# Kernel optimization log

Measured on AMD Instinct MI355X. Metric: run time of the kernel, lower is better.

Reference implementation:

```python
import jax, jax.numpy as jnp
import numpy as np

B, S, D = 2, 2048, 4096
H, KV, HD = 32, 8, 128
THETA = 10000.0


def rotate_half(x):
    x1, x2 = x[..., : HD // 2], x[..., HD // 2 :]
    return jnp.concatenate((-x2, x1), axis=-1)


def setup_inputs() -> dict:
    key = jax.random.key(0)
    ks = jax.random.split(key, 8)
    s = 1.0 / np.sqrt(D)
    return {
        "hidden_states": jax.random.normal(ks[0], (B, S, D), jnp.float32),
        "modality_indicators": jax.random.randint(ks[1], (B, S), 0, 2, jnp.int64 if jax.config.jax_enable_x64 else jnp.int32),
        "position_ids": jnp.arange(S, dtype=jnp.int32),
        "Wq": jax.random.normal(ks[2], (D, H * HD), jnp.float32) * s,
        "Wk0": jax.random.normal(ks[3], (D, KV * HD), jnp.float32) * s,
        "Wk1": jax.random.normal(ks[4], (D, KV * HD), jnp.float32) * s,
        "Wv0": jax.random.normal(ks[5], (D, KV * HD), jnp.float32) * s,
        "Wv1": jax.random.normal(ks[6], (D, KV * HD), jnp.float32) * s,
        "Wo": jax.random.normal(ks[7], (H * HD, D), jnp.float32) * s,
    }


def reference(hidden_states, modality_indicators, position_ids, Wq, Wk0, Wk1, Wv0, Wv1, Wo):
    x = hidden_states
    # Multiway (modality-routed) k/v projections: per-token select between two linears.
    sel = (modality_indicators == 1)[..., None]  # [B,S,1]
    q = x @ Wq                                   # [B,S,H*HD]
    k = jnp.where(sel, x @ Wk1, x @ Wk0)         # [B,S,KV*HD]
    v = jnp.where(sel, x @ Wv1, x @ Wv0)

    q = q.reshape(B, S, H, HD).transpose(0, 2, 1, 3)    # [B,H,S,HD]
    k = k.reshape(B, S, KV, HD).transpose(0, 2, 1, 3)   # [B,KV,S,HD]
    v = v.reshape(B, S, KV, HD).transpose(0, 2, 1, 3)

    # RoPE cache and application (emb = cat(freqs, freqs))
    inv_freq = 1.0 / (THETA ** (jnp.arange(0, HD, 2, dtype=jnp.float32) / HD))
    freqs = position_ids.astype(jnp.float32)[:, None] * inv_freq[None, :]   # [S,HD/2]
    emb = jnp.concatenate((freqs, freqs), axis=-1)                          # [S,HD]
    cos = jnp.cos(emb)[None, None, :, :]                                    # [1,1,S,HD]
    sin = jnp.sin(emb)[None, None, :, :]
    q = q * cos + rotate_half(q) * sin
    k = k * cos + rotate_half(k) * sin

    # GQA: repeat kv heads
    n_rep = H // KV
    k = jnp.repeat(k, n_rep, axis=1)  # [B,H,S,HD]
    v = jnp.repeat(v, n_rep, axis=1)

    scores = jnp.einsum("bhqd,bhkd->bhqk", q, k) / np.sqrt(HD)
    causal = jnp.tril(jnp.ones((S, S), dtype=bool))
    scores = jnp.where(causal[None, None], scores, jnp.finfo(scores.dtype).min)
    attn = jax.nn.softmax(scores, axis=-1)
    ctx = jnp.einsum("bhqk,bhkd->bhqd", attn, v)            # [B,H,S,HD]
    ctx = ctx.transpose(0, 2, 1, 3).reshape(B, S, H * HD)
    return ctx @ Wo
```

## Files before the change

### kernel.cpp

```cpp
#include <hip/hip_runtime.h>

typedef unsigned short u16;
typedef unsigned int   u32;
using bf16x8 = __attribute__((ext_vector_type(8))) __bf16;
using f32x4  = __attribute__((ext_vector_type(4))) float;
using f32x16 = __attribute__((ext_vector_type(16))) float;
using u32x4  = __attribute__((ext_vector_type(4))) unsigned int;


__device__ __forceinline__ u16 f2bf(float f) {
  u32 u = __builtin_bit_cast(u32, f);
  return (u16)((u + 0x7fffu + ((u >> 16) & 1u)) >> 16);
}
__device__ __forceinline__ float bf2f(u16 h) {
  return __builtin_bit_cast(float, (u32)h << 16);
}
__device__ __forceinline__ f32x4 mfma16(bf16x8 a, bf16x8 b, f32x4 c) {
  return __builtin_amdgcn_mfma_f32_16x16x32_bf16(a, b, c, 0, 0, 0);
}
__device__ __forceinline__ f32x16 mfma32(bf16x8 a, bf16x8 b, f32x16 c) {
  return __builtin_amdgcn_mfma_f32_32x32x16_bf16(a, b, c, 0, 0, 0);
}
__device__ __forceinline__ f32x16 zero16() {
  f32x16 z;
#pragma unroll
  for (int i = 0; i < 16; ++i) z[i] = 0.f;
  return z;
}
__device__ __forceinline__ void g2l16(const void* gp, void* lp) {
  __builtin_amdgcn_global_load_lds(
      (__attribute__((address_space(1))) void*)(void*)gp,
      (__attribute__((address_space(3))) void*)lp, 16, 0, 0);
}

__global__ void k_cvt(const float* __restrict__ in, u16* __restrict__ out, int n4) {
  int i = blockIdx.x * 256 + threadIdx.x;
  if (i >= n4) return;
  float4 v = ((const float4*)in)[i];
  ushort4 o;
  o.x = f2bf(v.x); o.y = f2bf(v.y); o.z = f2bf(v.z); o.w = f2bf(v.w);
  ((ushort4*)out)[i] = o;
}

__global__ void k_tcvt(const float* __restrict__ in, u16* __restrict__ out, int K, int N) {
  __shared__ u16 t[32][33];
  int n0 = blockIdx.x * 32, k0 = blockIdx.y * 32;
  int r = threadIdx.x >> 3, c4 = (threadIdx.x & 7) * 4;
  float4 v = *(const float4*)(in + (size_t)(k0 + r) * N + n0 + c4);
  t[c4 + 0][r] = f2bf(v.x);
  t[c4 + 1][r] = f2bf(v.y);
  t[c4 + 2][r] = f2bf(v.z);
  t[c4 + 3][r] = f2bf(v.w);
  __syncthreads();
  ushort4 o;
  o.x = t[r][c4 + 0]; o.y = t[r][c4 + 1]; o.z = t[r][c4 + 2]; o.w = t[r][c4 + 3];
  *(ushort4*)(out + (size_t)(n0 + r) * K + k0 + c4) = o;
}

#define TILE_BODY(T, VMLIT, DOSTAGE)                                         \
  {                                                                          \
    asm volatile("s_waitcnt vmcnt(" VMLIT ")" ::: "memory");                 \
    __builtin_amdgcn_s_barrier();                                            \
    __builtin_amdgcn_sched_barrier(0);                                       \
    const u16* base_ = lds + ((T) & 3) * 16384;                              \
    bf16x8 bfr[4], afr[4];                                                   \
    _Pragma("unroll")                                                        \
    for (int nf = 0; nf < 4; ++nf)                                           \
      bfr[nf] = *(const bf16x8*)(base_ + boff + nf * 512);                   \
    _Pragma("unroll")                                                        \
    for (int mf = 0; mf < 4; ++mf)                                           \
      afr[mf] = *(const bf16x8*)(base_ + aoff + mf * 512);                   \
    if (DOSTAGE) stage((T) + 3);                                             \
    __builtin_amdgcn_s_setprio(1);                                           \
    _Pragma("unroll")                                                        \
    for (int mf = 0; mf < 4; ++mf)                                           \
      _Pragma("unroll")                                                      \
      for (int nf = 0; nf < 4; ++nf)                                         \
        acc[mf][nf] = mfma16(afr[mf], bfr[nf], acc[mf][nf]);                 \
    __builtin_amdgcn_s_setprio(0);                                           \
    _Pragma("unroll")                                                        \
    for (int mf = 0; mf < 4; ++mf)                                           \
      afr[mf] = *(const bf16x8*)(base_ + aoff + (mf + 4) * 512);             \
    __builtin_amdgcn_s_setprio(1);                                           \
    _Pragma("unroll")                                                        \
    for (int mf = 0; mf < 4; ++mf)                                           \
      _Pragma("unroll")                                                      \
      for (int nf = 0; nf < 4; ++nf)                                         \
        acc[mf + 4][nf] = mfma16(afr[mf], bfr[nf], acc[mf + 4][nf]);         \
    __builtin_amdgcn_s_setprio(0);                                           \
  }

template <int MODE>
__global__ __launch_bounds__(512, 2) void k_gemm8(const u16* __restrict__ A, const u16* __restrict__ Bt,
                                                  void* __restrict__ Cp, int NH) {
  __shared__ u16 lds[4 * 16384];
  const int tid = threadIdx.x, wid = tid >> 6, l = tid & 63, g = l >> 4, li = l & 15;
  const int wr = wid >> 2, wc = wid & 3;
  const int bid = blockIdx.x;
  const int swz = (bid & 7) * 32 + (bid >> 3);
  const int m0 = (swz >> 4) * 256, n0 = (swz & 15) * 256;

  const int bo = wid * 2048 + l * 16;
  const int srow = bo >> 6;
  const int sgg = (l & 3) ^ ((l >> 3) & 3);
  const u16* ApA = A + (size_t)(m0 + srow) * 4096 + sgg * 8;
  const u16* ApB = Bt + (size_t)(n0 + srow) * 4096 + sgg * 8;

  auto stage = [&](int t) {
    const u16* a = ApA + t * 32;
    const u16* b = ApB + t * 32;
    u16* da = (u16*)lds + (t & 3) * 16384 + wid * 1024;
    u16* db = da + 8192;
    g2l16(a, da);
    g2l16(a + (size_t)16 * 4096, da + 512);
    g2l16(b, db);
    g2l16(b + (size_t)16 * 4096, db + 512);
  };

  const int lsl8 = (g ^ ((li >> 1) & 3)) * 8;
  const int aoff = (wr * 128 + li) * 32 + lsl8;
  const int boff = 8192 + (wc * 64 + li) * 32 + lsl8;

  const f32x4 vzero = {0.f, 0.f, 0.f, 0.f};
  f32x4 acc[8][4];
#pragma unroll
  for (int m = 0; m < 8; ++m)
#pragma unroll
    for (int n = 0; n < 4; ++n) acc[m][n] = vzero;

  stage(0); stage(1); stage(2);
  for (int t = 0; t < 125; ++t) TILE_BODY(t, "8", true);
  TILE_BODY(125, "8", false);
  TILE_BODY(126, "4", false);
  TILE_BODY(127, "0", false);

  (void)NH;
#pragma unroll
  for (int mf = 0; mf < 8; ++mf)
#pragma unroll
    for (int nf = 0; nf < 4; ++nf)
#pragma unroll
      for (int j = 0; j < 4; ++j) {
        int row = m0 + wr * 128 + mf * 16 + g * 4 + j;
        int col = n0 + wc * 64 + nf * 16 + li;
        float v = acc[mf][nf][j];
        if constexpr (MODE == 2) {
          ((float*)Cp)[(size_t)row * 4096 + col] = v;
        } else if constexpr (MODE == 1) {
          int b = row >> 11, s = row & 2047, h = col >> 7, d = col & 127;
          ((u16*)Cp)[(((size_t)(b * NH + h)) * 2048 + s) * 128 + d] = f2bf(v);
        } else {
          int b = row >> 11, s = row & 2047;
          int buf = col >> 10, hh = (col >> 7) & 7, d = col & 127;
          ((u16*)Cp)[(size_t)buf * 4194304 + (((size_t)(b * 8 + hh)) * 2048 + s) * 128 + d] = f2bf(v);
        }
      }
}

__global__ void k_ropeq(u16* __restrict__ Q, const int* __restrict__ pos) {
  int row = blockIdx.x * 4 + (threadIdx.x >> 6);
  int l = threadIdx.x & 63;
  int s = row & 2047;
  u16* p = Q + (size_t)row * 128;
  float x1 = bf2f(p[l]), x2 = bf2f(p[l + 64]);
  float ang = (float)pos[s] * expf((float)l * -0.14391156831212787f);
  float cs = cosf(ang), sn = sinf(ang);
  const float sc = 0.08838834764831845f;
  p[l] = f2bf((x1 * cs - x2 * sn) * sc);
  p[l + 64] = f2bf((x2 * cs + x1 * sn) * sc);
}

__global__ void k_kvprep(const u16* __restrict__ K0, const u16* __restrict__ K1,
                         const u16* __restrict__ V0, const u16* __restrict__ V1,
                         const int* __restrict__ mod, const int* __restrict__ pos,
                         u16* __restrict__ Kr, u16* __restrict__ Vt) {
  __shared__ u16 Vl[64][136];
  int blk = blockIdx.x;
  int st = blk & 31, kvh = (blk >> 5) & 7, b = blk >> 8;
  int s0 = st * 64;
  int tid = threadIdx.x, wid = tid >> 6, l = tid & 63;
  float invf = expf((float)l * -0.14391156831212787f);
  size_t slab = (size_t)(b * 8 + kvh) * 2048;
  for (int rr = 0; rr < 16; ++rr) {
    int r = wid * 16 + rr;
    int s = s0 + r;
    int sel = mod[b * 2048 + s];
    const u16* ks = (sel ? K1 : K0) + (slab + s) * 128;
    const u16* vs = (sel ? V1 : V0) + (slab + s) * 128;
    float ang = (float)pos[s] * invf;
    float cs = cosf(ang), sn = sinf(ang);
    float x1 = bf2f(ks[l]), x2 = bf2f(ks[l + 64]);
    u16* kd = Kr + (slab + s) * 128;
    kd[l] = f2bf(x1 * cs - x2 * sn);
    kd[l + 64] = f2bf(x2 * cs + x1 * sn);
    Vl[r][l] = vs[l];
    Vl[r][l + 64] = vs[l + 64];
  }
  __syncthreads();
  int d = tid >> 1, si0 = (tid & 1) * 32;
  u16* vd = Vt + ((size_t)(b * 8 + kvh) * 128 + d) * 2048 + s0 + si0;
#pragma unroll
  for (int k4 = 0; k4 < 8; ++k4) {
    ushort4 o;
    o.x = Vl[si0 + k4 * 4 + 0][d];
    o.y = Vl[si0 + k4 * 4 + 1][d];
    o.z = Vl[si0 + k4 * 4 + 2][d];
    o.w = Vl[si0 + k4 * 4 + 3][d];
    *(ushort4*)(vd + k4 * 4) = o;
  }
}

__global__ __launch_bounds__(256, 2) void k_attn(const u16* __restrict__ Q, const u16* __restrict__ Kr,
                                                 const u16* __restrict__ Vt, u16* __restrict__ ctx) {
  __shared__ u16 Kl[2 * 64 * 128];
  __shared__ u16 Vl[2 * 128 * 64];
  const int bh = blockIdx.x;
  const int qi = 15 - (int)blockIdx.y;
  const int b = bh >> 5, h = bh & 31, kvh = h >> 2;
  const int tid = threadIdx.x, w = tid >> 6, l = tid & 63;
  const int lo5 = l & 31, hi = l >> 5;
  const bool hib = hi != 0;
  const int q0 = qi * 128;
  const int qlane = q0 + w * 32 + lo5;
  const size_t kvslab = (size_t)(b * 8 + kvh) * 2048;
  const u16* Kg = Kr + kvslab * 128;
  const u16* Vg = Vt + kvslab * 128;

  auto stage = [&](int kt, int bi) {
#pragma unroll
    for (int i = 0; i < 4; ++i) {
      int c = w * 4 + i;
      int slot = c * 1024 + l * 16;
      {
        int row = slot >> 8;
        int inner = (slot & 255) ^ ((row & 7) << 4);
        g2l16((const char*)Kg + kt * 16384 + row * 256 + inner,
              (char*)Kl + bi * 16384 + c * 1024);
      }
      {
        int row = slot >> 7;
        int inner = (slot & 127) ^ ((row & 7) << 4);
        g2l16((const char*)Vg + (size_t)row * 4096 + kt * 128 + inner,
              (char*)Vl + bi * 16384 + c * 1024);
      }
    }
  };

  const u16* qrow = Q + ((size_t)bh * 2048 + qlane) * 128;
  bf16x8 qf[8];
#pragma unroll
  for (int kk = 0; kk < 8; ++kk) qf[kk] = *(const bf16x8*)(qrow + kk * 16 + hi * 8);

  f32x16 ot[4];
#pragma unroll
  for (int i = 0; i < 4; ++i) ot[i] = zero16();
  float m = -1e30f, ls = 0.f;
  const float L2E = 1.4426950408889634f;

  const int nkt = 2 * qi + 2;
  stage(0, 0);
  __syncthreads();
  int cur = 0;
  for (int kt = 0; kt < nkt; ++kt) {
    if (kt + 1 < nkt) stage(kt + 1, cur ^ 1);
    const char* kbase = (const char*)Kl + cur * 16384;
    const char* vbase = (const char*)Vl + cur * 16384;
    const int ktb = kt * 64;
    if (ktb <= q0 + w * 32 + 31) {
      f32x16 st[2];
      st[0] = zero16(); st[1] = zero16();
#pragma unroll
      for (int kk = 0; kk < 8; ++kk) {
        bf16x8 kfr[2];
#pragma unroll
        for (int mf = 0; mf < 2; ++mf) {
          int row = mf * 32 + lo5;
          kfr[mf] = *(const bf16x8*)(kbase + row * 256 + ((kk * 32 + hi * 16) ^ ((row & 7) << 4)));
        }
        __builtin_amdgcn_s_setprio(1);
        st[0] = mfma32(kfr[0], qf[kk], st[0]);
        st[1] = mfma32(kfr[1], qf[kk], st[1]);
        __builtin_amdgcn_s_setprio(0);
      }
      if (ktb + 63 > q0 + w * 32) {
#pragma unroll
        for (int mf = 0; mf < 2; ++mf)
#pragma unroll
          for (int r = 0; r < 16; ++r) {
            int kg = ktb + mf * 32 + (r & 3) + 8 * (r >> 2) + 4 * hi;
            if (kg > qlane) st[mf][r] = -3.0e38f;
          }
      }
      float t[16];
#pragma unroll
      for (int r = 0; r < 16; ++r) t[r] = fmaxf(st[0][r], st[1][r]);
#pragma unroll
      for (int s = 8; s >= 1; s >>= 1)
#pragma unroll
        for (int r = 0; r < s; ++r) t[r] = fmaxf(t[r], t[r + s]);
      float pmax = fmaxf(t[0], __shfl_xor(t[0], 32));
      if (!__all(pmax <= m + 8.f)) {
        float nm = fmaxf(m, pmax);
        float resc = exp2f((m - nm) * L2E);
        m = nm;
        ls *= resc;
#pragma unroll
        for (int i = 0; i < 4; ++i)
#pragma unroll
          for (int r = 0; r < 16; ++r) ot[i][r] *= resc;
      }
#pragma unroll
      for (int mf = 0; mf < 2; ++mf)
#pragma unroll
        for (int r = 0; r < 16; ++r) st[mf][r] = exp2f((st[mf][r] - m) * L2E);
      float u[16];
#pragma unroll
      for (int r = 0; r < 16; ++r) u[r] = st[0][r] + st[1][r];
#pragma unroll
      for (int s = 8; s >= 1; s >>= 1)
#pragma unroll
        for (int r = 0; r < s; ++r) u[r] += u[r + s];
      ls += u[0] + __shfl_xor(u[0], 32);
      u32 pkv[16];
#pragma unroll
      for (int mf = 0; mf < 2; ++mf)
#pragma unroll
        for (int tt = 0; tt < 8; ++tt) {
          u32 r;
          asm("v_cvt_pk_bf16_f32 %0, %1, %2" : "=v"(r) : "v"(st[mf][2 * tt]), "v"(st[mf][2 * tt + 1]));
          pkv[mf * 8 + tt] = r;
        }
      bf16x8 pfrag[4];
#pragma unroll
      for (int kk = 0; kk < 4; ++kk) {
        int c = (kk >> 1) * 8 + (kk & 1) * 4;
        u32 m0 = hib ? pkv[c + 2] : pkv[c + 0];
        u32 m1 = hib ? pkv[c + 3] : pkv[c + 1];
        u32 s0 = hib ? pkv[c + 0] : pkv[c + 2];
        u32 s1 = hib ? pkv[c + 1] : pkv[c + 3];
        u32 r0 = (u32)__shfl_xor((int)s0, 32);
        u32 r1 = (u32)__shfl_xor((int)s1, 32);
        u32x4 wv = {hib ? r0 : m0, hib ? r1 : m1, hib ? m0 : r0, hib ? m1 : r1};
        pfrag[kk] = __builtin_bit_cast(bf16x8, wv);
      }
#pragma unroll
      for (int mfV = 0; mfV < 4; ++mfV) {
        int row = mfV * 32 + lo5;
        const char* vb = vbase + row * 128;
        int sw = (row & 7) << 4;
        bf16x8 vf[4];
#pragma unroll
        for (int kk = 0; kk < 4; ++kk)
          vf[kk] = *(const bf16x8*)(vb + ((kk * 32 + hi * 16) ^ sw));
        __builtin_amdgcn_s_setprio(1);
#pragma unroll
        for (int kk = 0; kk < 4; ++kk) ot[mfV] = mfma32(vf[kk], pfrag[kk], ot[mfV]);
        __builtin_amdgcn_s_setprio(0);
      }
    }
    __syncthreads();
    cur ^= 1;
  }
  float inv = 1.0f / ls;
  u16* crow = ctx + ((size_t)(b * 2048) + qlane) * 4096 + h * 128;
#pragma unroll
  for (int mfV = 0; mfV < 4; ++mfV)
#pragma unroll
    for (int rq = 0; rq < 4; ++rq) {
      ushort4 o4;
      o4.x = f2bf(ot[mfV][rq * 4 + 0] * inv);
      o4.y = f2bf(ot[mfV][rq * 4 + 1] * inv);
      o4.z = f2bf(ot[mfV][rq * 4 + 2] * inv);
      o4.w = f2bf(ot[mfV][rq * 4 + 3] * inv);
      *(ushort4*)(crow + mfV * 32 + rq * 8 + hi * 4) = o4;
    }
}

extern "C" void kernel_launch(void* const* d_in, const int* in_sizes, int n_in,
                              void* d_out, int out_size, void* d_ws, size_t ws_size,
                              hipStream_t stream) {
  (void)in_sizes; (void)n_in; (void)out_size; (void)ws_size;
  const float* X   = (const float*)d_in[0];
  const int*   mod = (const int*)d_in[1];
  const int*   pos = (const int*)d_in[2];
  const float* Wq  = (const float*)d_in[3];
  const float* Wk0 = (const float*)d_in[4];
  const float* Wk1 = (const float*)d_in[5];
  const float* Wv0 = (const float*)d_in[6];
  const float* Wv1 = (const float*)d_in[7];
  const float* Wo  = (const float*)d_in[8];
  float* out = (float*)d_out;

  u16* p = (u16*)d_ws;
  auto take = [&](size_t n) { u16* r = p; p += n; return r; };
  u16* Xb   = take(16777216);
  u16* WqT  = take(16777216);
  u16* WoT  = take(16777216);
  u16* WkvT = take(16777216);
  u16* Qr   = take(16777216);
  u16* KV4  = take(16777216);
  u16* Kr  = WqT;
  u16* Vtr = WqT + 4194304;
  u16* ctx = Xb;

  k_cvt<<<dim3(16384), 256, 0, stream>>>(X, Xb, 4194304);
  k_tcvt<<<dim3(128, 128), 256, 0, stream>>>(Wq, WqT, 4096, 4096);
  k_tcvt<<<dim3(32, 128), 256, 0, stream>>>(Wk0, WkvT,               4096, 1024);
  k_tcvt<<<dim3(32, 128), 256, 0, stream>>>(Wk1, WkvT + 1 * 4194304, 4096, 1024);
  k_tcvt<<<dim3(32, 128), 256, 0, stream>>>(Wv0, WkvT + 2 * 4194304, 4096, 1024);
  k_tcvt<<<dim3(32, 128), 256, 0, stream>>>(Wv1, WkvT + 3 * 4194304, 4096, 1024);
  k_tcvt<<<dim3(128, 128), 256, 0, stream>>>(Wo, WoT, 4096, 4096);

  k_gemm8<1><<<dim3(256), 512, 0, stream>>>(Xb, WqT,  (void*)Qr,  32);
  k_gemm8<3><<<dim3(256), 512, 0, stream>>>(Xb, WkvT, (void*)KV4, 8);

  k_ropeq<<<dim3(32768), 256, 0, stream>>>(Qr, pos);
  k_kvprep<<<dim3(512), 256, 0, stream>>>(KV4, KV4 + 4194304, KV4 + 2 * 4194304,
                                          KV4 + 3 * 4194304, mod, pos, Kr, Vtr);

  k_attn<<<dim3(64, 16), 256, 0, stream>>>(Qr, Kr, Vtr, ctx);

  k_gemm8<2><<<dim3(256), 512, 0, stream>>>(ctx, WoT, (void*)out, 0);
}
```

Before: 581.5 us.

## Route tokens by modality into grouped KV GEMM and pair causal attention tiles

A prefix-scan kernel builds a per-batch permutation that groups tokens by modality, padded to 256-row tiles. A new grouped GEMM then computes only the selected K/V projection for each token instead of both and discarding half, which roughly halves the K/V projection FLOPs at the cost of gathered row loads and scattered stores. The attention kernel now processes two query tiles per block (p and 15-p) to balance causal work across blocks, halving the grid. The K tile LDS swizzle is also widened to 16 rows.

```diff
diff --git a/kernel.cpp b/kernel.cpp
--- a/kernel.cpp
+++ b/kernel.cpp
@@ -55,6 +55,35 @@
   ushort4 o;
   o.x = t[r][c4 + 0]; o.y = t[r][c4 + 1]; o.z = t[r][c4 + 2]; o.w = t[r][c4 + 3];
   *(ushort4*)(out + (size_t)(n0 + r) * K + k0 + c4) = o;
+}
+
+__global__ void k_scan(const int* __restrict__ mod, int* __restrict__ perm, int* __restrict__ meta) {
+  __shared__ int ps[1024];
+  const int b = blockIdx.x, t = threadIdx.x;
+  perm[b * 2304 + t] = -1;
+  perm[b * 2304 + 1024 + t] = -1;
+  if (t < 256) perm[b * 2304 + 2048 + t] = -1;
+  const int i0 = 2 * t, i1 = 2 * t + 1;
+  const int f0 = (mod[b * 2048 + i0] != 1) ? 1 : 0;
+  const int f1 = (mod[b * 2048 + i1] != 1) ? 1 : 0;
+  const int sum = f0 + f1;
+  ps[t] = sum;
+  __syncthreads();
+  for (int off = 1; off < 1024; off <<= 1) {
+    int v = (t >= off) ? ps[t - off] : 0;
+    __syncthreads();
+    ps[t] += v;
+    __syncthreads();
+  }
+  const int total0 = ps[1023];
+  const int excl = ps[t] - sum;
+  const int nt0 = (total0 + 255) >> 8;
+  const int off1 = nt0 * 256;
+  const int s0 = f0 ? excl : off1 + (i0 - excl);
+  const int s1 = f1 ? (excl + f0) : off1 + (i1 - (excl + f0));
+  perm[b * 2304 + s0] = i0;
+  perm[b * 2304 + s1] = i1;
+  if (t == 0) { meta[b * 2] = total0; meta[b * 2 + 1] = nt0; }
 }
 
 #define TILE_BODY(T, VMLIT, DOSTAGE)                                         \
@@ -149,10 +178,72 @@
         } else if constexpr (MODE == 1) {
           int b = row >> 11, s = row & 2047, h = col >> 7, d = col & 127;
           ((u16*)Cp)[(((size_t)(b * NH + h)) * 2048 + s) * 128 + d] = f2bf(v);
-        } else {
-          int b = row >> 11, s = row & 2047;
-          int buf = col >> 10, hh = (col >> 7) & 7, d = col & 127;
-          ((u16*)Cp)[(size_t)buf * 4194304 + (((size_t)(b * 8 + hh)) * 2048 + s) * 128 + d] = f2bf(v);
+        }
+      }
+}
+
+__global__ __launch_bounds__(512, 2) void k_gemmkv(const u16* __restrict__ Xb,
+                                                   const u16* __restrict__ B0, const u16* __restrict__ B1,
+                                                   const int* __restrict__ perm, const int* __restrict__ meta,
+                                                   u16* __restrict__ Ksel, u16* __restrict__ Vsel) {
+  __shared__ u16 lds[4 * 16384];
+  const int tid = threadIdx.x, wid = tid >> 6, l = tid & 63, g = l >> 4, li = l & 15;
+  const int wr = wid >> 2, wc = wid & 3;
+  const int bb = blockIdx.y / 9, tm = blockIdx.y % 9;
+  const int n0 = blockIdx.x * 256;
+  const int nt0 = meta[bb * 2 + 1];
+  const u16* Bt = (tm >= nt0) ? B1 : B0;
+
+  const int bo = wid * 2048 + l * 16;
+  const int srow = bo >> 6;
+  const int sgg = (l & 3) ^ ((l >> 3) & 3);
+  int t0 = perm[bb * 2304 + tm * 256 + srow];
+  int t1 = perm[bb * 2304 + tm * 256 + srow + 16];
+  if (t0 < 0) t0 = 0;
+  if (t1 < 0) t1 = 0;
+  const u16* ApA0 = Xb + ((size_t)bb * 2048 + t0) * 4096 + sgg * 8;
+  const u16* ApA1 = Xb + ((size_t)bb * 2048 + t1) * 4096 + sgg * 8;
+  const u16* ApB = Bt + (size_t)(n0 + srow) * 4096 + sgg * 8;
+
+  auto stage = [&](int t) {
+    u16* da = (u16*)lds + (t & 3) * 16384 + wid * 1024;
+    u16* db = da + 8192;
+    g2l16(ApA0 + t * 32, da);
+    g2l16(ApA1 + t * 32, da + 512);
+    g2l16(ApB + t * 32, db);
+    g2l16(ApB + (size_t)16 * 4096 + t * 32, db + 512);
+  };
+
+  const int lsl8 = (g ^ ((li >> 1) & 3)) * 8;
+  const int aoff = (wr * 128 + li) * 32 + lsl8;
+  const int boff = 8192 + (wc * 64 + li) * 32 + lsl8;
+
+  const f32x4 vzero = {0.f, 0.f, 0.f, 0.f};
+  f32x4 acc[8][4];
+#pragma unroll
+  for (int m = 0; m < 8; ++m)
+#pragma unroll
+    for (int n = 0; n < 4; ++n) acc[m][n] = vzero;
+
+  stage(0); stage(1); stage(2);
+  for (int t = 0; t < 125; ++t) TILE_BODY(t, "8", true);
+  TILE_BODY(125, "8", false);
+  TILE_BODY(126, "4", false);
+  TILE_BODY(127, "0", false);
+
+#pragma unroll
+  for (int mf = 0; mf < 8; ++mf)
+#pragma unroll
+    for (int nf = 0; nf < 4; ++nf)
+#pragma unroll
+      for (int j = 0; j < 4; ++j) {
+        int slot = tm * 256 + wr * 128 + mf * 16 + g * 4 + j;
+        int tok = perm[bb * 2304 + slot];
+        if (tok >= 0) {
+          int col = n0 + wc * 64 + nf * 16 + li;
+          int kv = col >> 10, hh = (col >> 7) & 7, d = col & 127;
+          u16* dst = (kv ? Vsel : Ksel) + (((size_t)(bb * 8 + hh)) * 2048 + tok) * 128 + d;
+          *dst = f2bf(acc[mf][nf][j]);
         }
       }
 }
@@ -170,9 +261,8 @@
   p[l + 64] = f2bf((x2 * cs + x1 * sn) * sc);
 }
 
-__global__ void k_kvprep(const u16* __restrict__ K0, const u16* __restrict__ K1,
-                         const u16* __restrict__ V0, const u16* __restrict__ V1,
-                         const int* __restrict__ mod, const int* __restrict__ pos,
+__global__ void k_kvprep(const u16* __restrict__ Ks, const u16* __restrict__ Vs,
+                         const int* __restrict__ pos,
                          u16* __restrict__ Kr, u16* __restrict__ Vt) {
   __shared__ u16 Vl[64][136];
   int blk = blockIdx.x;
@@ -184,9 +274,8 @@
   for (int rr = 0; rr < 16; ++rr) {
     int r = wid * 16 + rr;
     int s = s0 + r;
-    int sel = mod[b * 2048 + s];
-    const u16* ks = (sel ? K1 : K0) + (slab + s) * 128;
-    const u16* vs = (sel ? V1 : V0) + (slab + s) * 128;
+    const u16* ks = Ks + (slab + s) * 128;
+    const u16* vs = Vs + (slab + s) * 128;
     float ang = (float)pos[s] * invf;
     float cs = cosf(ang), sn = sinf(ang);
     float x1 = bf2f(ks[l]), x2 = bf2f(ks[l + 64]);
@@ -215,16 +304,15 @@
   __shared__ u16 Kl[2 * 64 * 128];
   __shared__ u16 Vl[2 * 128 * 64];
   const int bh = blockIdx.x;
-  const int qi = 15 - (int)blockIdx.y;
+  const int p = blockIdx.y;
   const int b = bh >> 5, h = bh & 31, kvh = h >> 2;
   const int tid = threadIdx.x, w = tid >> 6, l = tid & 63;
   const int lo5 = l & 31, hi = l >> 5;
   const bool hib = hi != 0;
-  const int q0 = qi * 128;
-  const int qlane = q0 + w * 32 + lo5;
   const size_t kvslab = (size_t)(b * 8 + kvh) * 2048;
   const u16* Kg = Kr + kvslab * 128;
   const u16* Vg = Vt + kvslab * 128;
+  const float L2E = 1.4426950408889634f;
 
   auto stage = [&](int kt, int bi) {
 #pragma unroll
@@ -233,7 +321,7 @@
       int slot = c * 1024 + l * 16;
       {
         int row = slot >> 8;
-        int inner = (slot & 255) ^ ((row & 7) << 4);
+        int inner = (slot & 255) ^ ((row & 15) << 4);
         g2l16((const char*)Kg + kt * 16384 + row * 256 + inner,
               (char*)Kl + bi * 16384 + c * 1024);
       }
@@ -246,134 +334,138 @@
     }
   };
 
-  const u16* qrow = Q + ((size_t)bh * 2048 + qlane) * 128;
-  bf16x8 qf[8];
-#pragma unroll
-  for (int kk = 0; kk < 8; ++kk) qf[kk] = *(const bf16x8*)(qrow + kk * 16 + hi * 8);
-
-  f32x16 ot[4];
-#pragma unroll
-  for (int i = 0; i < 4; ++i) ot[i] = zero16();
-  float m = -1e30f, ls = 0.f;
-  const float L2E = 1.4426950408889634f;
-
-  const int nkt = 2 * qi + 2;
-  stage(0, 0);
-  __syncthreads();
-  int cur = 0;
-  for (int kt = 0; kt < nkt; ++kt) {
-    if (kt + 1 < nkt) stage(kt + 1, cur ^ 1);
-    const char* kbase = (const char*)Kl + cur * 16384;
-    const char* vbase = (const char*)Vl + cur * 16384;
-    const int ktb = kt * 64;
-    if (ktb <= q0 + w * 32 + 31) {
-      f32x16 st[2];
-      st[0] = zero16(); st[1] = zero16();
-#pragma unroll
-      for (int kk = 0; kk < 8; ++kk) {
-        bf16x8 kfr[2];
-#pragma unroll
-        for (int mf = 0; mf < 2; ++mf) {
-          int row = mf * 32 + lo5;
-          kfr[mf] = *(const bf16x8*)(kbase + row * 256 + ((kk * 32 + hi * 16) ^ ((row & 7) << 4)));
-        }
-        __builtin_amdgcn_s_setprio(1);
-        st[0] = mfma32(kfr[0], qf[kk], st[0]);
-        st[1] = mfma32(kfr[1], qf[kk], st[1]);
-        __builtin_amdgcn_s_setprio(0);
+  for (int hf = 0; hf < 2; ++hf) {
+    const int qi = hf ? (15 - p) : p;
+    const int q0 = qi * 128;
+    const int qlane = q0 + w * 32 + lo5;
+    const u16* qrow = Q + ((size_t)bh * 2048 + qlane) * 128;
+    bf16x8 qf[8];
+#pragma unroll
+    for (int kk = 0; kk < 8; ++kk) qf[kk] = *(const bf16x8*)(qrow + kk * 16 + hi * 8);
+
+    f32x16 ot[4];
+#pragma unroll
+    for (int i = 0; i < 4; ++i) ot[i] = zero16();
+    float m = -1e30f, ls = 0.f;
+
+    const int nkt = 2 * qi + 2;
+    stage(0, 0);
+    __syncthreads();
+    int cur = 0;
+    for (int kt = 0; kt < nkt; ++kt) {
+      if (kt + 1 < nkt) stage(kt + 1, cur ^ 1);
+      const char* kbase = (const char*)Kl + cur * 16384;
+      const char* vbase = (const char*)Vl + cur * 16384;
+      const int ktb = kt * 64;
+      if (ktb <= q0 + w * 32 + 31) {
+        f32x16 st[2];
+        st[0] = zero16(); st[1] = zero16();
+#pragma unroll
+        for (int kk = 0; kk < 8; ++kk) {
+          bf16x8 kfr[2];
+#pragma unroll
+          for (int mf = 0; mf < 2; ++mf) {
+            int row = mf * 32 + lo5;
+            kfr[mf] = *(const bf16x8*)(kbase + row * 256 + ((kk * 32 + hi * 16) ^ ((row & 15) << 4)));
+          }
+          __builtin_amdgcn_s_setprio(1);
+          st[0] = mfma32(kfr[0], qf[kk], st[0]);
+          st[1] = mfma32(kfr[1], qf[kk], st[1]);
+          __builtin_amdgcn_s_setprio(0);
+        }
+        if (ktb + 63 > q0 + w * 32) {
+#pragma unroll
+          for (int mf = 0; mf < 2; ++mf)
+#pragma unroll
+            for (int r = 0; r < 16; ++r) {
+              int kg = ktb + mf * 32 + (r & 3) + 8 * (r >> 2) + 4 * hi;
+              if (kg > qlane) st[mf][r] = -3.0e38f;
+            }
+        }
+        float t[16];
+#pragma unroll
+        for (int r = 0; r < 16; ++r) t[r] = fmaxf(st[0][r], st[1][r]);
+#pragma unroll
+        for (int s = 8; s >= 1; s >>= 1)
+#pragma unroll
+          for (int r = 0; r < s; ++r) t[r] = fmaxf(t[r], t[r + s]);
+        float pmax = fmaxf(t[0], __shfl_xor(t[0], 32));
+        if (!__all(pmax <= m + 8.f)) {
+          float nm = fmaxf(m, pmax);
+          float resc = exp2f((m - nm) * L2E);
+          m = nm;
+          ls *= resc;
+#pragma unroll
+          for (int i = 0; i < 4; ++i)
+#pragma unroll
+            for (int r = 0; r < 16; ++r) ot[i][r] *= resc;
+        }
+#pragma unroll
+        for (int mf = 0; mf < 2; ++mf)
+#pragma unroll
+          for (int r = 0; r < 16; ++r) st[mf][r] = exp2f((st[mf][r] - m) * L2E);
+        float u[16];
+#pragma unroll
+        for (int r = 0; r < 16; ++r) u[r] = st[0][r] + st[1][r];
+#pragma unroll
+        for (int s = 8; s >= 1; s >>= 1)
+#pragma unroll
+          for (int r = 0; r < s; ++r) u[r] += u[r + s];
+        ls += u[0] + __shfl_xor(u[0], 32);
+        u32 pkv[16];
+#pragma unroll
+        for (int mf = 0; mf < 2; ++mf)
+#pragma unroll
+          for (int tt = 0; tt < 8; ++tt) {
+            u32 r;
+            asm("v_cvt_pk_bf16_f32 %0, %1, %2" : "=v"(r) : "v"(st[mf][2 * tt]), "v"(st[mf][2 * tt + 1]));
+            pkv[mf * 8 + tt] = r;
+          }
+        bf16x8 pfrag[4];
+#pragma unroll
+        for (int kk = 0; kk < 4; ++kk) {
+          int c = (kk >> 1) * 8 + (kk & 1) * 4;
+          u32 m0 = hib ? pkv[c + 2] : pkv[c + 0];
+          u32 m1 = hib ? pkv[c + 3] : pkv[c + 1];
+          u32 s0 = hib ? pkv[c + 0] : pkv[c + 2];
+          u32 s1 = hib ? pkv[c + 1] : pkv[c + 3];
+          u32 r0 = (u32)__shfl_xor((int)s0, 32);
+          u32 r1 = (u32)__shfl_xor((int)s1, 32);
+          u32x4 wv = {hib ? r0 : m0, hib ? r1 : m1, hib ? m0 : r0, hib ? m1 : r1};
+          pfrag[kk] = __builtin_bit_cast(bf16x8, wv);
+        }
+#pragma unroll
+        for (int mfV = 0; mfV < 4; ++mfV) {
+          int row = mfV * 32 + lo5;
+          const char* vb = vbase + row * 128;
+          int sw = (row & 7) << 4;
+          bf16x8 vf[4];
+#pragma unroll
+          for (int kk = 0; kk < 4; ++kk)
+            vf[kk] = *(const bf16x8*)(vb + ((kk * 32 + hi * 16) ^ sw));
+          __builtin_amdgcn_s_setprio(1);
+#pragma unroll
+          for (int kk = 0; kk < 4; ++kk) ot[mfV] = mfma32(vf[kk], pfrag[kk], ot[mfV]);
+          __builtin_amdgcn_s_setprio(0);
+        }
       }
-      if (ktb + 63 > q0 + w * 32) {
-#pragma unroll
-        for (int mf = 0; mf < 2; ++mf)
-#pragma unroll
-          for (int r = 0; r < 16; ++r) {
-            int kg = ktb + mf * 32 + (r & 3) + 8 * (r >> 2) + 4 * hi;
-            if (kg > qlane) st[mf][r] = -3.0e38f;
-          }
+      __syncthreads();
+      cur ^= 1;
+    }
+    float inv = 1.0f / ls;
+    u16* crow = ctx + ((size_t)(b * 2048) + qlane) * 4096 + h * 128;
+#pragma unroll
+    for (int mfV = 0; mfV < 4; ++mfV)
+#pragma unroll
+      for (int rq = 0; rq < 4; ++rq) {
+        ushort4 o4;
+        o4.x = f2bf(ot[mfV][rq * 4 + 0] * inv);
+        o4.y = f2bf(ot[mfV][rq * 4 + 1] * inv);
+        o4.z = f2bf(ot[mfV][rq * 4 + 2] * inv);
+        o4.w = f2bf(ot[mfV][rq * 4 + 3] * inv);
+        *(ushort4*)(crow + mfV * 32 + rq * 8 + hi * 4) = o4;
       }
-      float t[16];
-#pragma unroll
-      for (int r = 0; r < 16; ++r) t[r] = fmaxf(st[0][r], st[1][r]);
-#pragma unroll
-      for (int s = 8; s >= 1; s >>= 1)
-#pragma unroll
-        for (int r = 0; r < s; ++r) t[r] = fmaxf(t[r], t[r + s]);
-      float pmax = fmaxf(t[0], __shfl_xor(t[0], 32));
-      if (!__all(pmax <= m + 8.f)) {
-        float nm = fmaxf(m, pmax);
-        float resc = exp2f((m - nm) * L2E);
-        m = nm;
-        ls *= resc;
-#pragma unroll
-        for (int i = 0; i < 4; ++i)
-#pragma unroll
-          for (int r = 0; r < 16; ++r) ot[i][r] *= resc;
-      }
-#pragma unroll
-      for (int mf = 0; mf < 2; ++mf)
-#pragma unroll
-        for (int r = 0; r < 16; ++r) st[mf][r] = exp2f((st[mf][r] - m) * L2E);
-      float u[16];
-#pragma unroll
-      for (int r = 0; r < 16; ++r) u[r] = st[0][r] + st[1][r];
-#pragma unroll
-      for (int s = 8; s >= 1; s >>= 1)
-#pragma unroll
-        for (int r = 0; r < s; ++r) u[r] += u[r + s];
-      ls += u[0] + __shfl_xor(u[0], 32);
-      u32 pkv[16];
-#pragma unroll
-      for (int mf = 0; mf < 2; ++mf)
-#pragma unroll
-        for (int tt = 0; tt < 8; ++tt) {
-          u32 r;
-          asm("v_cvt_pk_bf16_f32 %0, %1, %2" : "=v"(r) : "v"(st[mf][2 * tt]), "v"(st[mf][2 * tt + 1]));
-          pkv[mf * 8 + tt] = r;
-        }
-      bf16x8 pfrag[4];
-#pragma unroll
-      for (int kk = 0; kk < 4; ++kk) {
-        int c = (kk >> 1) * 8 + (kk & 1) * 4;
-        u32 m0 = hib ? pkv[c + 2] : pkv[c + 0];
-        u32 m1 = hib ? pkv[c + 3] : pkv[c + 1];
-        u32 s0 = hib ? pkv[c + 0] : pkv[c + 2];
-        u32 s1 = hib ? pkv[c + 1] : pkv[c + 3];
-        u32 r0 = (u32)__shfl_xor((int)s0, 32);
-        u32 r1 = (u32)__shfl_xor((int)s1, 32);
-        u32x4 wv = {hib ? r0 : m0, hib ? r1 : m1, hib ? m0 : r0, hib ? m1 : r1};
-        pfrag[kk] = __builtin_bit_cast(bf16x8, wv);
-      }
-#pragma unroll
-      for (int mfV = 0; mfV < 4; ++mfV) {
-        int row = mfV * 32 + lo5;
-        const char* vb = vbase + row * 128;
-        int sw = (row & 7) << 4;
-        bf16x8 vf[4];
-#pragma unroll
-        for (int kk = 0; kk < 4; ++kk)
-          vf[kk] = *(const bf16x8*)(vb + ((kk * 32 + hi * 16) ^ sw));
-        __builtin_amdgcn_s_setprio(1);
-#pragma unroll
-        for (int kk = 0; kk < 4; ++kk) ot[mfV] = mfma32(vf[kk], pfrag[kk], ot[mfV]);
-        __builtin_amdgcn_s_setprio(0);
-      }
-    }
-    __syncthreads();
-    cur ^= 1;
   }
-  float inv = 1.0f / ls;
-  u16* crow = ctx + ((size_t)(b * 2048) + qlane) * 4096 + h * 128;
-#pragma unroll
-  for (int mfV = 0; mfV < 4; ++mfV)
-#pragma unroll
-    for (int rq = 0; rq < 4; ++rq) {
-      ushort4 o4;
-      o4.x = f2bf(ot[mfV][rq * 4 + 0] * inv);
-      o4.y = f2bf(ot[mfV][rq * 4 + 1] * inv);
-      o4.z = f2bf(ot[mfV][rq * 4 + 2] * inv);
-      o4.w = f2bf(ot[mfV][rq * 4 + 3] * inv);
-      *(ushort4*)(crow + mfV * 32 + rq * 8 + hi * 4) = o4;
-    }
 }
 
 extern "C" void kernel_launch(void* const* d_in, const int* in_sizes, int n_in,
@@ -393,32 +485,36 @@
 
   u16* p = (u16*)d_ws;
   auto take = [&](size_t n) { u16* r = p; p += n; return r; };
-  u16* Xb   = take(16777216);
-  u16* WqT  = take(16777216);
-  u16* WoT  = take(16777216);
-  u16* WkvT = take(16777216);
-  u16* Qr   = take(16777216);
-  u16* KV4  = take(16777216);
+  u16* Xb    = take(16777216);
+  u16* WqT   = take(16777216);
+  u16* WoT   = take(16777216);
+  u16* Wkv0T = take(8388608);
+  u16* Wkv1T = take(8388608);
+  u16* Qr    = take(16777216);
+  u16* Ksel  = take(4194304);
+  u16* Vsel  = take(4194304);
+  int* perm  = (int*)take(9216);
+  int* meta  = (int*)take(64);
   u16* Kr  = WqT;
   u16* Vtr = WqT + 4194304;
   u16* ctx = Xb;
 
   k_cvt<<<dim3(16384), 256, 0, stream>>>(X, Xb, 4194304);
+  k_scan<<<dim3(2), 1024, 0, stream>>>(mod, perm, meta);
   k_tcvt<<<dim3(128, 128), 256, 0, stream>>>(Wq, WqT, 4096, 4096);
-  k_tcvt<<<dim3(32, 128), 256, 0, stream>>>(Wk0, WkvT,               4096, 1024);
-  k_tcvt<<<dim3(32, 128), 256, 0, stream>>>(Wk1, WkvT + 1 * 4194304, 4096, 1024);
-  k_tcvt<<<dim3(32, 128), 256, 0, stream>>>(Wv0, WkvT + 2 * 4194304, 4096, 1024);
-  k_tcvt<<<dim3(32, 128), 256, 0, stream>>>(Wv1, WkvT + 3 * 4194304, 4096, 1024);
+  k_tcvt<<<dim3(32, 128), 256, 0, stream>>>(Wk0, Wkv0T,                4096, 1024);
+  k_tcvt<<<dim3(32, 128), 256, 0, stream>>>(Wv0, Wkv0T + 1024 * 4096,  4096, 1024);
+  k_tcvt<<<dim3(32, 128), 256, 0, stream>>>(Wk1, Wkv1T,                4096, 1024);
+  k_tcvt<<<dim3(32, 128), 256, 0, stream>>>(Wv1, Wkv1T + 1024 * 4096,  4096, 1024);
   k_tcvt<<<dim3(128, 128), 256, 0, stream>>>(Wo, WoT, 4096, 4096);
 
-  k_gemm8<1><<<dim3(256), 512, 0, stream>>>(Xb, WqT,  (void*)Qr,  32);
-  k_gemm8<3><<<dim3(256), 512, 0, stream>>>(Xb, WkvT, (void*)KV4, 8);
+  k_gemm8<1><<<dim3(256), 512, 0, stream>>>(Xb, WqT, (void*)Qr, 32);
+  k_gemmkv<<<dim3(8, 18), 512, 0, stream>>>(Xb, Wkv0T, Wkv1T, perm, meta, Ksel, Vsel);
 
   k_ropeq<<<dim3(32768), 256, 0, stream>>>(Qr, pos);
-  k_kvprep<<<dim3(512), 256, 0, stream>>>(KV4, KV4 + 4194304, KV4 + 2 * 4194304,
-                                          KV4 + 3 * 4194304, mod, pos, Kr, Vtr);
-
-  k_attn<<<dim3(64, 16), 256, 0, stream>>>(Qr, Kr, Vtr, ctx);
+  k_kvprep<<<dim3(512), 256, 0, stream>>>(Ksel, Vsel, pos, Kr, Vtr);
+
+  k_attn<<<dim3(64, 8), 256, 0, stream>>>(Qr, Kr, Vtr, ctx);
 
   k_gemm8<2><<<dim3(256), 512, 0, stream>>>(ctx, WoT, (void*)out, 0);
 }
```

Measured after the change: 585.1 us. Within noise of the previous version (+0.6%).
